# Kernel optimization log

Measured on AMD Instinct MI355X. Metric: run time of the kernel, lower is better.

## Reference

```python
import jax, jax.numpy as jnp
import numpy as np
from math import sqrt

B, N, D = 16, 4096, 128
M = 64 * 24  # mem_size_per_joint * num_joints


def setup_inputs() -> dict:
    key = jax.random.key(0)
    kx, km = jax.random.split(key)
    x = jax.random.normal(kx, (B, N, D), dtype=jnp.float32)
    mem = jax.random.normal(km, (1, D, M), dtype=jnp.float32)  # N(0,1) init as in torch
    return {"x": x, "mem": mem}


def reference(x, mem):
    # x: (B, N, D); mem: (1, D, M)
    d = x.shape[-1]
    w = mem[0]  # (D, M)
    # logits = bmm(m_key (B,M,D), x_ (B,D,N)) / sqrt(D)  -> (B, M, N)
    logits = jnp.einsum('dm,bnd->bmn', w, x) / sqrt(d)
    # softmax over the memory axis (dim=1 in torch layout)
    attn = jax.nn.softmax(logits, axis=1)  # (B, M, N)
    # x_new = bmm(m (B,D,M), attn) -> (B,D,N); output permuted to (B,N,D)
    out = jnp.einsum('dm,bmn->bnd', w, attn)
    return out
```

## Files before the change

kernel.cpp:

```cpp
#include <hip/hip_runtime.h>
#include <math.h>


#define Bdim 16
#define Ndim 4096
#define Ddim 128
#define Mdim 1536
#define NT 128
#define NTHREADS 512
#define NSESS 24
#define NFRAG 24576

typedef __attribute__((ext_vector_type(8)))  _Float16 f16x8;
typedef __attribute__((ext_vector_type(16))) float    f32x16;

union H2 { _Float16 h[2]; unsigned u; };
union F8 { unsigned u[4]; f16x8 v; };

__global__ void jamb_prep(const float* __restrict__ w,
                          _Float16* __restrict__ wt,
                          _Float16* __restrict__ wd) {
    const int tid = blockIdx.x * 256 + threadIdx.x;
    const float SC = 0.12751742957f;
    if (tid < NFRAG) {
        const int f    = tid;
        const int l    = f & 63;
        const int fs   = f >> 6;
        const int ks   = fs & 7;
        const int mt   = fs >> 3;
        const int m    = mt * 32 + (l & 31);
        const int d0   = ks * 16 + (l >> 5) * 8;
        f16x8 pk;
        #pragma unroll
        for (int j = 0; j < 8; ++j)
            pk[j] = (_Float16)(w[(size_t)(d0 + j) * Mdim + m] * SC);
        *(f16x8*)&wt[(size_t)f * 8] = pk;
    } else {
        const int f    = tid - NFRAG;
        const int l    = f & 63;
        const int fs   = f >> 6;
        const int dt   = fs & 3;
        const int km   = fs >> 2;
        const int d    = dt * 32 + (l & 31);
        const int m0   = km * 16 + (l >> 5) * 8;
        const float* src = w + (size_t)d * Mdim + m0;
        const float4 v0 = *(const float4*)src;
        const float4 v1 = *(const float4*)(src + 4);
        f16x8 pk;
        pk[0] = (_Float16)v0.x; pk[1] = (_Float16)v0.y;
        pk[2] = (_Float16)v0.z; pk[3] = (_Float16)v0.w;
        pk[4] = (_Float16)v1.x; pk[5] = (_Float16)v1.y;
        pk[6] = (_Float16)v1.z; pk[7] = (_Float16)v1.w;
        *(f16x8*)&wd[(size_t)f * 8] = pk;
    }
}

static __device__ __forceinline__ void glds16(const void* g, void* l) {
    __builtin_amdgcn_global_load_lds(
        (const __attribute__((address_space(1))) unsigned*)g,
        (__attribute__((address_space(3))) unsigned*)l, 16, 0, 0);
}

__global__ __launch_bounds__(NTHREADS, 4)
void jamb_mfma_kernel(const float* __restrict__ x,
                      const _Float16* __restrict__ wt,
                      const _Float16* __restrict__ wd,
                      float* __restrict__ out) {
    __shared__ __align__(16) unsigned char smem[65536];
    __shared__ float sred[4][32];

    const int t   = threadIdx.x;
    const int w   = t >> 6;
    const int l   = t & 63;
    const int l31 = l & 31;
    const int hi  = l >> 5;
    const int wm  = w >> 2;
    const int u   = w & 3;

    const int blk   = blockIdx.x;
    const int b     = blk >> 5;
    const int nbase = (blk & 31) * NT;

    f16x8 bx[8];
    {
        const float* xr = x + (size_t)(b * Ndim + nbase + u * 32 + l31) * Ddim;
        #pragma unroll
        for (int ks = 0; ks < 8; ++ks) {
            const float* s = xr + ks * 16 + hi * 8;
            const float4 v0 = *(const float4*)s;
            const float4 v1 = *(const float4*)(s + 4);
            f16x8 pk;
            pk[0] = (_Float16)v0.x; pk[1] = (_Float16)v0.y;
            pk[2] = (_Float16)v0.z; pk[3] = (_Float16)v0.w;
            pk[4] = (_Float16)v1.x; pk[5] = (_Float16)v1.y;
            pk[6] = (_Float16)v1.z; pk[7] = (_Float16)v1.w;
            bx[ks] = pk;
        }
    }

    const char* wtc = (const char*)wt;
    const char* wdc = (const char*)wd;
    const int lane16 = l * 16;
    const int chunk  = w * 2048;

    auto stage = [&](int q) {
        const int bs = (q & 1) * 16384;
        const int gq = q * 16384;
        glds16(wtc + gq + chunk + 0    + lane16, smem + bs + chunk + 0);
        glds16(wtc + gq + chunk + 1024 + lane16, smem + bs + chunk + 1024);
        glds16(wdc + gq + chunk + 0    + lane16, smem + 32768 + bs + chunk + 0);
        glds16(wdc + gq + chunk + 1024 + lane16, smem + 32768 + bs + chunk + 1024);
    };

    float ssum = 0.f;
    f32x16 c[4];
    #pragma unroll
    for (int dt = 0; dt < 4; ++dt) c[dt] = (f32x16)(0.f);

    stage(0);
    __syncthreads();

    #pragma unroll 1
    for (int q = 0; q < NSESS; ++q) {
        if (q + 1 < NSESS) stage(q + 1);
        const _Float16* WTl = (const _Float16*)(smem + (q & 1) * 16384);
        const _Float16* WDl = (const _Float16*)(smem + 32768 + (q & 1) * 16384);

        f32x16 acc = (f32x16)(0.f);
        #pragma unroll
        for (int ks = 0; ks < 8; ++ks) {
            const f16x8 fh = *(const f16x8*)(WTl + ((wm * 8 + ks) * 64 + l) * 8);
            acc = __builtin_amdgcn_mfma_f32_32x32x16_f16(fh, bx[ks], acc, 0, 0, 0);
        }
        unsigned Wg[4][2];
        #pragma unroll
        for (int g = 0; g < 4; ++g) {
            const float e0 = exp2f(acc[4 * g + 0]);
            const float e1 = exp2f(acc[4 * g + 1]);
            const float e2 = exp2f(acc[4 * g + 2]);
            const float e3 = exp2f(acc[4 * g + 3]);
            ssum += (e0 + e1) + (e2 + e3);
            H2 pa; pa.h[0] = (_Float16)e0; pa.h[1] = (_Float16)e1;
            H2 pb; pb.h[0] = (_Float16)e2; pb.h[1] = (_Float16)e3;
            Wg[g][0] = pa.u; Wg[g][1] = pb.u;
        }
        F8 pf[2];
        #pragma unroll
        for (int k2 = 0; k2 < 2; ++k2) {
            unsigned a0 = Wg[2 * k2][0], b0 = Wg[2 * k2 + 1][0];
            unsigned a1 = Wg[2 * k2][1], b1 = Wg[2 * k2 + 1][1];
            asm volatile("v_permlane32_swap_b32 %0, %1" : "+v"(a0), "+v"(b0));
            asm volatile("v_permlane32_swap_b32 %0, %1" : "+v"(a1), "+v"(b1));
            pf[k2].u[0] = a0; pf[k2].u[1] = a1;
            pf[k2].u[2] = b0; pf[k2].u[3] = b1;
        }

        #pragma unroll
        for (int k2 = 0; k2 < 2; ++k2) {
            const int kk = 2 * wm + k2;
            #pragma unroll
            for (int dt = 0; dt < 4; ++dt) {
                const f16x8 a = *(const f16x8*)(WDl + ((kk * 4 + dt) * 64 + l) * 8);
                c[dt] = __builtin_amdgcn_mfma_f32_32x32x16_f16(a, pf[k2].v, c[dt], 0, 0, 0);
            }
        }
        __syncthreads();
    }

    ssum += __shfl_xor(ssum, 32, 64);
    if (wm == 1) {
        if (hi == 0) sred[u][l31] = ssum;
        float* cx = (float*)smem + u * 4096;
        #pragma unroll
        for (int dt = 0; dt < 4; ++dt) {
            #pragma unroll
            for (int g = 0; g < 4; ++g) {
                float4 v;
                v.x = c[dt][4 * g + 0]; v.y = c[dt][4 * g + 1];
                v.z = c[dt][4 * g + 2]; v.w = c[dt][4 * g + 3];
                *(float4*)(cx + ((dt * 4 + g) * 64 + l) * 4) = v;
            }
        }
    }
    __syncthreads();
    if (wm == 0) {
        const float inv = 1.f / (ssum + sred[u][l31]);
        const float* cx = (const float*)smem + u * 4096;
        float* ob = out + (size_t)(b * Ndim + nbase + u * 32 + l31) * Ddim;
        #pragma unroll
        for (int dt = 0; dt < 4; ++dt) {
            #pragma unroll
            for (int g = 0; g < 4; ++g) {
                const float4 pc = *(const float4*)(cx + ((dt * 4 + g) * 64 + l) * 4);
                float4 o;
                o.x = (c[dt][4 * g + 0] + pc.x) * inv;
                o.y = (c[dt][4 * g + 1] + pc.y) * inv;
                o.z = (c[dt][4 * g + 2] + pc.z) * inv;
                o.w = (c[dt][4 * g + 3] + pc.w) * inv;
                *(float4*)(ob + dt * 32 + g * 8 + hi * 4) = o;
            }
        }
    }
}

extern "C" void kernel_launch(void* const* d_in, const int* in_sizes, int n_in,
                              void* d_out, int out_size, void* d_ws, size_t ws_size,
                              hipStream_t stream) {
    const float* x = (const float*)d_in[0];
    const float* w = (const float*)d_in[1];
    float* out = (float*)d_out;
    (void)in_sizes; (void)n_in; (void)out_size; (void)ws_size;

    _Float16* wt = (_Float16*)d_ws;
    _Float16* wd = wt + Ddim * Mdim;

    jamb_prep<<<dim3((2 * NFRAG) / 256), dim3(256), 0, stream>>>(w, wt, wd);
    jamb_mfma_kernel<<<dim3((Bdim * Ndim) / NT), dim3(NTHREADS), 0, stream>>>(x, wt, wd, out);
}
```

Baseline: 156.9 us.

## Shrink tiles, load logits weights from global, software-pipeline QK MFMA, transpose prep via LDS

The main kernel now uses 64-row tiles with 256 threads, so there are twice as many blocks. The first-GEMM weight fragments are read straight from global memory (L2) into registers, and only the second-GEMM weights are staged in LDS. The first GEMM for the next memory chunk is computed after the current chunk's second GEMM, so its loads overlap the exp and accumulate work. The prep kernel now transposes the weights through shared memory, which makes its global reads coalesced. The cost is more register pressure (an occupancy hint of 3 instead of 4), and the weights are reloaded from global for every block.

Measured after the change: 192.8 us. +22.9%, slower.

```diff
diff --git a/kernel.cpp b/kernel.cpp
--- a/kernel.cpp
+++ b/kernel.cpp
@@ -6,10 +6,9 @@
 #define Ndim 4096
 #define Ddim 128
 #define Mdim 1536
-#define NT 128
-#define NTHREADS 512
+#define NT 64
+#define NTHREADS 256
 #define NSESS 24
-#define NFRAG 24576
 
 typedef __attribute__((ext_vector_type(8)))  _Float16 f16x8;
 typedef __attribute__((ext_vector_type(16))) float    f32x16;
@@ -17,41 +16,47 @@
 union H2 { _Float16 h[2]; unsigned u; };
 union F8 { unsigned u[4]; f16x8 v; };
 
-__global__ void jamb_prep(const float* __restrict__ w,
-                          _Float16* __restrict__ wt,
-                          _Float16* __restrict__ wd) {
-    const int tid = blockIdx.x * 256 + threadIdx.x;
+__global__ __launch_bounds__(256)
+void jamb_prep(const float* __restrict__ w,
+               _Float16* __restrict__ wt,
+               _Float16* __restrict__ wd) {
+    __shared__ float ts[32 * 132];
+    const int t  = threadIdx.x;
+    const int mt = blockIdx.x;
+    #pragma unroll
+    for (int i = 0; i < 16; ++i) {
+        const int f = t + i * 256;
+        const int d = f >> 5;
+        const int m = f & 31;
+        ts[m * 132 + d] = w[(size_t)d * Mdim + mt * 32 + m];
+    }
+    __syncthreads();
     const float SC = 0.12751742957f;
-    if (tid < NFRAG) {
-        const int f    = tid;
-        const int l    = f & 63;
-        const int fs   = f >> 6;
-        const int ks   = fs & 7;
-        const int mt   = fs >> 3;
-        const int m    = mt * 32 + (l & 31);
-        const int d0   = ks * 16 + (l >> 5) * 8;
+    #pragma unroll
+    for (int h = 0; h < 2; ++h) {
+        const int fr = t + h * 256;
+        const int l  = fr & 63;
+        const int ks = fr >> 6;
+        const int m  = l & 31;
+        const int d0 = ks * 16 + (l >> 5) * 8;
         f16x8 pk;
         #pragma unroll
         for (int j = 0; j < 8; ++j)
-            pk[j] = (_Float16)(w[(size_t)(d0 + j) * Mdim + m] * SC);
-        *(f16x8*)&wt[(size_t)f * 8] = pk;
-    } else {
-        const int f    = tid - NFRAG;
-        const int l    = f & 63;
-        const int fs   = f >> 6;
-        const int dt   = fs & 3;
-        const int km   = fs >> 2;
+            pk[j] = (_Float16)(ts[m * 132 + d0 + j] * SC);
+        *(f16x8*)&wt[(size_t)((mt * 8 + ks) * 64 + l) * 8] = pk;
+    }
+    #pragma unroll
+    for (int h = 0; h < 2; ++h) {
+        const int l    = t & 63;
+        const int dt   = t >> 6;
+        const int km   = mt * 2 + h;
         const int d    = dt * 32 + (l & 31);
-        const int m0   = km * 16 + (l >> 5) * 8;
-        const float* src = w + (size_t)d * Mdim + m0;
-        const float4 v0 = *(const float4*)src;
-        const float4 v1 = *(const float4*)(src + 4);
+        const int mloc = h * 16 + (l >> 5) * 8;
         f16x8 pk;
-        pk[0] = (_Float16)v0.x; pk[1] = (_Float16)v0.y;
-        pk[2] = (_Float16)v0.z; pk[3] = (_Float16)v0.w;
-        pk[4] = (_Float16)v1.x; pk[5] = (_Float16)v1.y;
-        pk[6] = (_Float16)v1.z; pk[7] = (_Float16)v1.w;
-        *(f16x8*)&wd[(size_t)f * 8] = pk;
+        #pragma unroll
+        for (int j = 0; j < 8; ++j)
+            pk[j] = (_Float16)ts[(mloc + j) * 132 + d];
+        *(f16x8*)&wd[(size_t)((km * 4 + dt) * 64 + l) * 8] = pk;
     }
 }
 
@@ -61,25 +66,25 @@
         (__attribute__((address_space(3))) unsigned*)l, 16, 0, 0);
 }
 
-__global__ __launch_bounds__(NTHREADS, 4)
+__global__ __launch_bounds__(NTHREADS, 3)
 void jamb_mfma_kernel(const float* __restrict__ x,
                       const _Float16* __restrict__ wt,
                       const _Float16* __restrict__ wd,
                       float* __restrict__ out) {
-    __shared__ __align__(16) unsigned char smem[65536];
-    __shared__ float sred[4][32];
+    __shared__ __align__(16) _Float16 wdbuf[2][8192];
+    __shared__ float sred[2][2][32];
 
     const int t   = threadIdx.x;
     const int w   = t >> 6;
     const int l   = t & 63;
     const int l31 = l & 31;
     const int hi  = l >> 5;
-    const int wm  = w >> 2;
-    const int u   = w & 3;
+    const int wm  = w >> 1;
+    const int u   = w & 1;
 
     const int blk   = blockIdx.x;
-    const int b     = blk >> 5;
-    const int nbase = (blk & 31) * NT;
+    const int b     = blk >> 6;
+    const int nbase = (blk & 63) * NT;
 
     f16x8 bx[8];
     {
@@ -98,18 +103,17 @@
         }
     }
 
-    const char* wtc = (const char*)wt;
-    const char* wdc = (const char*)wd;
+    const f16x8* WTg = (const f16x8*)wt;
+    const char*  wdc = (const char*)wd;
     const int lane16 = l * 16;
-    const int chunk  = w * 2048;
 
     auto stage = [&](int q) {
-        const int bs = (q & 1) * 16384;
-        const int gq = q * 16384;
-        glds16(wtc + gq + chunk + 0    + lane16, smem + bs + chunk + 0);
-        glds16(wtc + gq + chunk + 1024 + lane16, smem + bs + chunk + 1024);
-        glds16(wdc + gq + chunk + 0    + lane16, smem + 32768 + bs + chunk + 0);
-        glds16(wdc + gq + chunk + 1024 + lane16, smem + 32768 + bs + chunk + 1024);
+        char* dst = (char*)&wdbuf[q & 1][0] + w * 4096;
+        const char* src = wdc + q * 16384 + w * 4096;
+        glds16(src + 0    + lane16, dst + 0);
+        glds16(src + 1024 + lane16, dst + 1024);
+        glds16(src + 2048 + lane16, dst + 2048);
+        glds16(src + 3072 + lane16, dst + 3072);
     };
 
     float ssum = 0.f;
@@ -118,20 +122,26 @@
     for (int dt = 0; dt < 4; ++dt) c[dt] = (f32x16)(0.f);
 
     stage(0);
+    f32x16 acc = (f32x16)(0.f);
+    {
+        #pragma unroll
+        for (int ks = 0; ks < 8; ++ks) {
+            const f16x8 fh = WTg[(size_t)((0 + wm) * 8 + ks) * 64 + l];
+            acc = __builtin_amdgcn_mfma_f32_32x32x16_f16(fh, bx[ks], acc, 0, 0, 0);
+        }
+    }
     __syncthreads();
 
     #pragma unroll 1
     for (int q = 0; q < NSESS; ++q) {
-        if (q + 1 < NSESS) stage(q + 1);
-        const _Float16* WTl = (const _Float16*)(smem + (q & 1) * 16384);
-        const _Float16* WDl = (const _Float16*)(smem + 32768 + (q & 1) * 16384);
-
-        f32x16 acc = (f32x16)(0.f);
-        #pragma unroll
-        for (int ks = 0; ks < 8; ++ks) {
-            const f16x8 fh = *(const f16x8*)(WTl + ((wm * 8 + ks) * 64 + l) * 8);
-            acc = __builtin_amdgcn_mfma_f32_32x32x16_f16(fh, bx[ks], acc, 0, 0, 0);
-        }
+        f16x8 fhn[8];
+        if (q + 1 < NSESS) {
+            stage(q + 1);
+            #pragma unroll
+            for (int ks = 0; ks < 8; ++ks)
+                fhn[ks] = WTg[(size_t)((2 * (q + 1) + wm) * 8 + ks) * 64 + l];
+        }
+
         unsigned Wg[4][2];
         #pragma unroll
         for (int g = 0; g < 4; ++g) {
@@ -155,22 +165,34 @@
             pf[k2].u[2] = b0; pf[k2].u[3] = b1;
         }
 
-        #pragma unroll
-        for (int k2 = 0; k2 < 2; ++k2) {
-            const int kk = 2 * wm + k2;
-            #pragma unroll
-            for (int dt = 0; dt < 4; ++dt) {
-                const f16x8 a = *(const f16x8*)(WDl + ((kk * 4 + dt) * 64 + l) * 8);
-                c[dt] = __builtin_amdgcn_mfma_f32_32x32x16_f16(a, pf[k2].v, c[dt], 0, 0, 0);
+        {
+            const _Float16* WDl = &wdbuf[q & 1][0];
+            #pragma unroll
+            for (int k2 = 0; k2 < 2; ++k2) {
+                const int kk = 2 * wm + k2;
+                #pragma unroll
+                for (int dt = 0; dt < 4; ++dt) {
+                    const f16x8 a = *(const f16x8*)(WDl + ((kk * 4 + dt) * 64 + l) * 8);
+                    c[dt] = __builtin_amdgcn_mfma_f32_32x32x16_f16(a, pf[k2].v, c[dt], 0, 0, 0);
+                }
             }
         }
+
+        if (q + 1 < NSESS) {
+            f32x16 an = (f32x16)(0.f);
+            #pragma unroll
+            for (int ks = 0; ks < 8; ++ks)
+                an = __builtin_amdgcn_mfma_f32_32x32x16_f16(fhn[ks], bx[ks], an, 0, 0, 0);
+            acc = an;
+        }
         __syncthreads();
     }
 
     ssum += __shfl_xor(ssum, 32, 64);
+    if (hi == 0) sred[wm][u][l31] = ssum;
+    float* cxbase = (float*)&wdbuf[0][0];
     if (wm == 1) {
-        if (hi == 0) sred[u][l31] = ssum;
-        float* cx = (float*)smem + u * 4096;
+        float* cx = cxbase + u * 4096;
         #pragma unroll
         for (int dt = 0; dt < 4; ++dt) {
             #pragma unroll
@@ -184,8 +206,8 @@
     }
     __syncthreads();
     if (wm == 0) {
-        const float inv = 1.f / (ssum + sred[u][l31]);
-        const float* cx = (const float*)smem + u * 4096;
+        const float inv = 1.f / (sred[0][u][l31] + sred[1][u][l31]);
+        const float* cx = cxbase + u * 4096;
         float* ob = out + (size_t)(b * Ndim + nbase + u * 32 + l31) * Ddim;
         #pragma unroll
         for (int dt = 0; dt < 4; ++dt) {
@@ -214,6 +236,6 @@
     _Float16* wt = (_Float16*)d_ws;
     _Float16* wd = wt + Ddim * Mdim;
 
-    jamb_prep<<<dim3((2 * NFRAG) / 256), dim3(256), 0, stream>>>(w, wt, wd);
+    jamb_prep<<<dim3(48), dim3(256), 0, stream>>>(w, wt, wd);
     jamb_mfma_kernel<<<dim3((Bdim * Ndim) / NT), dim3(NTHREADS), 0, stream>>>(x, wt, wd, out);
 }
```
